# Optimization experiments

Hardware: AMD Instinct MI355X
Metric: run time of the kernel (lower is better)

## Reference

```python
import jax, jax.numpy as jnp
import numpy as np

B = 16384
D1 = 256
D2 = 256
D_FF = 1024
N_BINS = 16
TAIL = 3.0
MIN_VAL = 1e-3
MIN_TOTAL = N_BINS * MIN_VAL
TAIL_CONST = float(np.log(np.exp(1.0 - MIN_VAL) - 1.0))
D_OUT = (3 * N_BINS - 1) * D2  # 12032


def setup_inputs() -> dict:
    key = jax.random.key(0)
    ks = jax.random.split(key, 8)
    s = lambda fan: 1.0 / np.sqrt(fan)
    return {
        'x1': jax.random.normal(ks[0], (B, D1), jnp.float32),
        'x2': jax.random.normal(ks[1], (B, D2), jnp.float32),
        'W0': jax.random.normal(ks[2], (D1, D_FF), jnp.float32) * s(D1),
        'b0': jnp.zeros((D_FF,), jnp.float32),
        'W1': jax.random.normal(ks[3], (D_FF, D_FF), jnp.float32) * s(D_FF),
        'b1': jnp.zeros((D_FF,), jnp.float32),
        'W2': jax.random.normal(ks[4], (D_FF, D_OUT), jnp.float32) * s(D_FF),
        'b2': jnp.zeros((D_OUT,), jnp.float32),
    }


def _rqs_forward(x, wu, hu, du):
    # x: [B, D2]; wu, hu: [B, D2, N_BINS]; du: [B, D2, N_BINS-1]
    widths = MIN_VAL + (1.0 - MIN_TOTAL) * jax.nn.softmax(wu, axis=-1)
    heights = MIN_VAL + (1.0 - MIN_TOTAL) * jax.nn.softmax(hu, axis=-1)
    cw = jnp.cumsum(widths, axis=-1)
    cw = jnp.concatenate([jnp.zeros_like(cw[..., :1]), cw], axis=-1)
    cw = 2.0 * TAIL * cw - TAIL  # x bin edges in [-TAIL, TAIL], [B,D2,N_BINS+1]
    ch = jnp.cumsum(heights, axis=-1)
    ch = jnp.concatenate([jnp.zeros_like(ch[..., :1]), ch], axis=-1)
    ch = 2.0 * TAIL * ch - TAIL  # y bin edges
    w = cw[..., 1:] - cw[..., :-1]
    h = ch[..., 1:] - ch[..., :-1]
    # boundary derivatives padded so softplus(TAIL_CONST)+MIN_VAL == 1 (linear tails)
    pad = jnp.full_like(du[..., :1], TAIL_CONST)
    d = MIN_VAL + jax.nn.softplus(jnp.concatenate([pad, du, pad], axis=-1))  # [B,D2,N_BINS+1]
    inside = (x > -TAIL) & (x < TAIL)
    xc = jnp.clip(x, -TAIL, TAIL)
    # data-dependent bin search against interior edges
    idx = jnp.sum((xc[..., None] >= cw[..., 1:-1]).astype(jnp.int32), axis=-1)  # [B,D2]
    take = lambda a: jnp.take_along_axis(a, idx[..., None], axis=-1)[..., 0]
    xk = take(cw[..., :-1]); yk = take(ch[..., :-1])
    wk = take(w); hk = take(h)
    dk = take(d[..., :-1]); dk1 = take(d[..., 1:])
    sk = hk / wk
    theta = (xc - xk) / wk
    t1m = theta * (1.0 - theta)
    denom = sk + (dk + dk1 - 2.0 * sk) * t1m
    y = yk + hk * (sk * theta * theta + dk * t1m) / denom
    deriv = sk * sk * (dk1 * theta * theta + 2.0 * sk * t1m + dk * (1.0 - theta) ** 2) / (denom * denom)
    y = jnp.where(inside, y, x)            # identity tails
    logdet = jnp.where(inside, jnp.log(deriv), 0.0)
    return y, jnp.sum(logdet, axis=-1)     # [B,D2], [B]


def reference(x1, x2, W0, b0, W1, b1, W2, b2):
    # conditioner MLP: x1 -> spline parameters
    hdn = jax.nn.relu(x1 @ W0 + b0)
    hdn = jax.nn.relu(hdn @ W1 + b1)
    p = (hdn @ W2 + b2).reshape(-1, D2, 3 * N_BINS - 1)
    wu = p[..., :N_BINS]
    hu = p[..., N_BINS:2 * N_BINS]
    du = p[..., 2 * N_BINS:]
    y2, logdet = _rqs_forward(x2, wu, hu, du)
    return y2, logdet
```

## Files before the change

### kernel.cpp

```cpp
#include <hip/hip_runtime.h>
#include <math.h>

using u16 = unsigned short;
using bf16x8 = __attribute__((ext_vector_type(8))) short;
using f32x4  = __attribute__((ext_vector_type(4))) float;

#define DEV static __device__ __forceinline__

DEV u16 f2bf(float f) {
  union { float f; unsigned u; } v; v.f = f;
  unsigned u = v.u + 0x7fffu + ((v.u >> 16) & 1u);
  return (u16)(u >> 16);
}

DEV void gload16(const void* g, void* l) {
  __builtin_amdgcn_global_load_lds(
      (const __attribute__((address_space(1))) void*)g,
      (__attribute__((address_space(3))) void*)l, 16, 0, 0);
}

__global__ void k_conv_bf16(const float* __restrict__ in, u16* __restrict__ out, int n) {
  int i = blockIdx.x * 256 + threadIdx.x;
  if (i < n) out[i] = f2bf(in[i]);
}

__global__ void k_transconv(const float* __restrict__ in, u16* __restrict__ out,
                            int K, int Nin, int Nout, int pack) {
  __shared__ float t[32][33];
  int kb = blockIdx.x * 32, nb = blockIdx.y * 32;
  int tx = threadIdx.x & 31, ty = threadIdx.x >> 5;
  #pragma unroll
  for (int i = 0; i < 4; ++i) {
    int k = kb + ty + i * 8;
    int no = nb + tx;
    float v = 0.f;
    if (k < K && no < Nout) {
      if (pack) {
        int r = no % 48;
        if (r < 47) v = in[(size_t)k * Nin + (no / 48) * 47 + r];
      } else {
        v = in[(size_t)k * Nin + no];
      }
    }
    t[ty + i * 8][tx] = v;
  }
  __syncthreads();
  #pragma unroll
  for (int i = 0; i < 4; ++i) {
    int no = nb + ty + i * 8;
    int k = kb + tx;
    if (no < Nout && k < K) out[(size_t)no * K + k] = f2bf(t[tx][ty + i * 8]);
  }
}

__global__ __launch_bounds__(256)
void k_gemm_relu(const u16* __restrict__ A, const u16* __restrict__ Bt,
                 const float* __restrict__ bias, u16* __restrict__ C,
                 int N, int K) {
  constexpr int BM = 128, BN = 128, BK = 32;
  __shared__ __align__(16) u16 lds[(BM + BN) * BK];
  int tid = threadIdx.x, w = tid >> 6, lane = tid & 63;
  int bn = blockIdx.x, bm = blockIdx.y;
  int brow = bm * BM, bcol = bn * BN;
  int wm = w >> 1, wn = w & 1;
  int fr = lane & 15, fg = lane >> 4;
  f32x4 acc[4][4];
  #pragma unroll
  for (int i = 0; i < 4; ++i)
    #pragma unroll
    for (int j = 0; j < 4; ++j) acc[i][j] = (f32x4){0.f, 0.f, 0.f, 0.f};

  constexpr int ACH = BM * BK / 8;
  constexpr int CALLS = (BM + BN) * BK / 8 / 64;

  for (int kt = 0; kt < K; kt += BK) {
    for (int j = 0; j * 4 + w < CALLS; ++j) {
      int cb = (j * 4 + w) * 64;
      int c = cb + lane;
      const u16* g;
      if (c < ACH) {
        int row = c >> 2, c8 = c & 3;
        g = A + (size_t)(brow + row) * K + kt + c8 * 8;
      } else {
        int b = c - ACH;
        int nn = b >> 2, c8 = b & 3;
        g = Bt + (size_t)(bcol + nn) * K + kt + c8 * 8;
      }
      gload16(g, &lds[cb * 8]);
    }
    asm volatile("s_waitcnt vmcnt(0)" ::: "memory");
    __syncthreads();

    const u16* Al = lds;
    const u16* Bl = lds + BM * BK;
    bf16x8 af[4], bfr[4];
    #pragma unroll
    for (int mi = 0; mi < 4; ++mi)
      af[mi] = *(const bf16x8*)&Al[(wm * 64 + mi * 16 + fr) * BK + fg * 8];
    #pragma unroll
    for (int ni = 0; ni < 4; ++ni)
      bfr[ni] = *(const bf16x8*)&Bl[(wn * 64 + ni * 16 + fr) * BK + fg * 8];
    #pragma unroll
    for (int mi = 0; mi < 4; ++mi)
      #pragma unroll
      for (int ni = 0; ni < 4; ++ni)
        acc[mi][ni] = __builtin_amdgcn_mfma_f32_16x16x32_bf16(af[mi], bfr[ni], acc[mi][ni], 0, 0, 0);
    __syncthreads();
  }

  #pragma unroll
  for (int ni = 0; ni < 4; ++ni) {
    int col = bcol + wn * 64 + ni * 16 + fr;
    float bb = bias[col];
    #pragma unroll
    for (int mi = 0; mi < 4; ++mi) {
      #pragma unroll
      for (int q = 0; q < 4; ++q) {
        int row = brow + wm * 64 + mi * 16 + fg * 4 + q;
        float vv = acc[mi][ni][q] + bb;
        C[(size_t)row * N + col] = f2bf(vv > 0.f ? vv : 0.f);
      }
    }
  }
}

__global__ __launch_bounds__(256, 3)
void k_gemm3_fused(const u16* __restrict__ A, const u16* __restrict__ Bt,
                   const float* __restrict__ b2, const float* __restrict__ x2,
                   float* __restrict__ y2, float* __restrict__ ldpart) {
  extern __shared__ char smem[];
  const int tid = threadIdx.x, w = tid >> 6, lane = tid & 63;
  const int wm = w >> 1, wn = w & 1;
  const int fr = lane & 15, fg = lane >> 4;

  const int bid = blockIdx.x;
  const int bm = bid >> 6;
  const int bn = ((bid & 7) << 3) | ((bid >> 3) & 7);
  const int brow = bm * 128;

  const int csrc = (tid & 3) ^ ((tid >> 3) & 3);
  const u16* gA0 = A + (size_t)(brow + (tid >> 2)) * 1024 + csrc * 8;
  const u16* gB0 = Bt + (size_t)(bn * 192 + (tid >> 2)) * 1024 + csrc * 8;

#define ISSUE_ALL(t1) {                                               \
    const size_t ko_ = (size_t)(t1) * 32;                             \
    char* p_ = smem + ((t1) & 1) * 20480 + tid * 16;                  \
    gload16(gA0 + ko_, p_);                                           \
    gload16(gA0 + 65536 + ko_, p_ + 4096);                            \
    gload16(gB0 + ko_, p_ + 8192);                                    \
    gload16(gB0 + 65536 + ko_, p_ + 12288);                           \
    gload16(gB0 + 131072 + ko_, p_ + 16384); }

  const int sc = ((fg ^ ((fr >> 1) & 3)) << 4);

  f32x4 acc[4][6];
  #pragma unroll
  for (int m = 0; m < 4; ++m)
    #pragma unroll
    for (int n = 0; n < 6; ++n) acc[m][n] = (f32x4){0.f, 0.f, 0.f, 0.f};

  ISSUE_ALL(0);
  asm volatile("s_waitcnt vmcnt(0)" ::: "memory");
  __syncthreads();

  for (int t = 0; t < 32; ++t) {
    if (t < 31) ISSUE_ALL(t + 1);
    const char* Ab = smem + (t & 1) * 20480;
    const char* Bb = Ab + 8192;
    bf16x8 b[6];
    #pragma unroll
    for (int n = 0; n < 6; ++n)
      b[n] = *(const bf16x8*)(Bb + (wn * 96 + n * 16 + fr) * 64 + sc);
    __builtin_amdgcn_s_setprio(1);
    #pragma unroll
    for (int m = 0; m < 4; ++m) {
      bf16x8 a = *(const bf16x8*)(Ab + (wm * 64 + m * 16 + fr) * 64 + sc);
      #pragma unroll
      for (int n = 0; n < 6; ++n)
        acc[m][n] = __builtin_amdgcn_mfma_f32_16x16x32_bf16(a, b[n], acc[m][n], 0, 0, 0);
    }
    __builtin_amdgcn_s_setprio(0);
    asm volatile("s_waitcnt vmcnt(0)" ::: "memory");
    __syncthreads();
  }

  float* ldacc = (float*)(smem + 50176);
  float* fl = (float*)smem;
  #pragma unroll
  for (int rh = 0; rh < 2; ++rh) {
    if (wm == rh) {
      #pragma unroll
      for (int m = 0; m < 4; ++m)
        #pragma unroll
        for (int n = 0; n < 6; ++n) {
          const int g = wn * 2 + (n >= 3 ? 1 : 0);
          const int ci = (n % 3) * 16 + fr;
          #pragma unroll
          for (int q = 0; q < 4; ++q)
            fl[g * 3136 + (m * 16 + fg * 4 + q) * 49 + ci] = acc[m][n][q];
        }
    }
    __syncthreads();
    {
      const int g = tid >> 6, r = tid & 63;
      const float* pr = fl + g * 3136 + r * 49;
      const int grow = brow + rh * 64 + r;
      const int d2 = bn * 4 + g;
      const float* bb = b2 + (size_t)d2 * 47;

      float wv[16], hv[16];
      #pragma unroll
      for (int j = 0; j < 16; ++j) wv[j] = pr[j] + bb[j];
      #pragma unroll
      for (int j = 0; j < 16; ++j) hv[j] = pr[16 + j] + bb[16 + j];

      float x = x2[(size_t)grow * 256 + d2];
      float xc = fminf(fmaxf(x, -3.f), 3.f);

      float mw = wv[0];
      #pragma unroll
      for (int j = 1; j < 16; ++j) mw = fmaxf(mw, wv[j]);
      float sw = 0.f;
      #pragma unroll
      for (int j = 0; j < 16; ++j) { wv[j] = __expf(wv[j] - mw); sw += wv[j]; }
      float scw = 0.984f / sw;

      float mh = hv[0];
      #pragma unroll
      for (int j = 1; j < 16; ++j) mh = fmaxf(mh, hv[j]);
      float sh = 0.f;
      #pragma unroll
      for (int j = 0; j < 16; ++j) { hv[j] = __expf(hv[j] - mh); sh += hv[j]; }
      float sch = 0.984f / sh;

      int idx = 0;
      float xk = -3.f, cum = 0.f;
      #pragma unroll
      for (int i = 1; i <= 15; ++i) {
        cum += 0.001f + wv[i - 1] * scw;
        float cwi = 6.f * cum - 3.f;
        if (xc >= cwi) { idx = i; xk = cwi; }
      }
      float yk = -3.f, cumh = 0.f;
      #pragma unroll
      for (int i = 1; i <= 15; ++i) {
        cumh += 0.001f + hv[i - 1] * sch;
        float chi = 6.f * cumh - 3.f;
        if (i == idx) yk = chi;
      }
      float wk = 1.f, hk = 1.f;
      #pragma unroll
      for (int i = 0; i < 16; ++i) {
        if (i == idx) {
          wk = 6.f * (0.001f + wv[i] * scw);
          hk = 6.f * (0.001f + hv[i] * sch);
        }
      }
      float dk = 1.f, dk1 = 1.f;
      #pragma unroll
      for (int i = 1; i <= 15; ++i) {
        float u = pr[32 + i - 1] + bb[32 + i - 1];
        float e = __expf(u);
        float dd = 0.001f + (u > 15.f ? u : log1pf(e));
        if (i == idx) dk = dd;
        if (i == idx + 1) dk1 = dd;
      }

      float sk = hk / wk;
      float th = (xc - xk) / wk;
      float om = 1.f - th;
      float t1m = th * om;
      float den = sk + (dk + dk1 - 2.f * sk) * t1m;
      float y = yk + hk * (sk * th * th + dk * t1m) / den;
      float deriv = sk * sk * (dk1 * th * th + 2.f * sk * t1m + dk * om * om) / (den * den);
      bool inside = (x > -3.f) && (x < 3.f);
      float yout = inside ? y : x;
      float ld = inside ? __logf(deriv) : 0.f;

      y2[(size_t)grow * 256 + d2] = yout;
      ldacc[(rh * 64 + r) * 4 + g] = ld;
    }
    __syncthreads();
  }

  if (tid < 128) {
    float s = ldacc[tid * 4] + ldacc[tid * 4 + 1] + ldacc[tid * 4 + 2] + ldacc[tid * 4 + 3];
    ldpart[(size_t)bn * 16384 + brow + tid] = s;
  }
}

__global__ void k_reduce_ld(const float* __restrict__ part, float* __restrict__ out) {
  int r = blockIdx.x * 256 + threadIdx.x;
  float s = 0.f;
  for (int j = 0; j < 64; ++j) s += part[(size_t)j * 16384 + r];
  out[r] = s;
}

extern "C" void kernel_launch(void* const* d_in, const int* in_sizes, int n_in,
                              void* d_out, int out_size, void* d_ws, size_t ws_size,
                              hipStream_t stream) {
  const float* x1 = (const float*)d_in[0];
  const float* x2 = (const float*)d_in[1];
  const float* W0 = (const float*)d_in[2];
  const float* b0 = (const float*)d_in[3];
  const float* W1 = (const float*)d_in[4];
  const float* b1 = (const float*)d_in[5];
  const float* W2 = (const float*)d_in[6];
  const float* b2 = (const float*)d_in[7];
  float* y2 = (float*)d_out;
  float* logdet = y2 + (size_t)16384 * 256;

  char* ws = (char*)d_ws;
  u16* W2t = (u16*)ws;
  u16* W0t = (u16*)(ws + 25165824);
  u16* W1t = (u16*)(ws + 25165824 + 524288);
  u16* x1b = (u16*)(ws + 27787264);
  float* ldp = (float*)(ws + 27787264);
  u16* h1  = (u16*)(ws + 36175872);
  u16* h2  = (u16*)(ws + 69730304);

  hipFuncSetAttribute((const void*)k_gemm3_fused,
                      hipFuncAttributeMaxDynamicSharedMemorySize, 52224);

  k_conv_bf16<<<16384, 256, 0, stream>>>(x1, x1b, 16384 * 256);
  k_transconv<<<dim3(8, 32), 256, 0, stream>>>(W0, W0t, 256, 1024, 1024, 0);
  k_transconv<<<dim3(32, 32), 256, 0, stream>>>(W1, W1t, 1024, 1024, 1024, 0);
  k_transconv<<<dim3(32, 384), 256, 0, stream>>>(W2, W2t, 1024, 12032, 12288, 1);

  k_gemm_relu<<<dim3(8, 128), 256, 0, stream>>>(x1b, W0t, b0, h1, 1024, 256);
  k_gemm_relu<<<dim3(8, 128), 256, 0, stream>>>(h1, W1t, b1, h2, 1024, 1024);
  k_gemm3_fused<<<8192, 256, 52224, stream>>>(h2, W2t, b2, x2, y2, ldp);
  k_reduce_ld<<<64, 256, 0, stream>>>(ldp, logdet);
}
```

Measured before the change: 747.3 us.

## Triple-buffer the fused output GEMM main loop with partial vmcnt waits

Replaces the double-buffered K loop of the fused third GEMM with a three-stage LDS ring. Each step issues loads two tiles ahead and waits with vmcnt(5) instead of draining all outstanding loads, so global-to-LDS transfers overlap more with MFMA work. Raw s_barrier calls plus sched_barrier replace __syncthreads. LDS grows to 60KB and launch bounds drop from 3 to 2 blocks per CU, which trades occupancy for deeper prefetch.

```diff
diff --git a/kernel.cpp b/kernel.cpp
--- a/kernel.cpp
+++ b/kernel.cpp
@@ -124,7 +124,7 @@
   }
 }
 
-__global__ __launch_bounds__(256, 3)
+__global__ __launch_bounds__(256, 2)
 void k_gemm3_fused(const u16* __restrict__ A, const u16* __restrict__ Bt,
                    const float* __restrict__ b2, const float* __restrict__ x2,
                    float* __restrict__ y2, float* __restrict__ ldpart) {
@@ -142,9 +142,9 @@
   const u16* gA0 = A + (size_t)(brow + (tid >> 2)) * 1024 + csrc * 8;
   const u16* gB0 = Bt + (size_t)(bn * 192 + (tid >> 2)) * 1024 + csrc * 8;
 
-#define ISSUE_ALL(t1) {                                               \
+#define STAGE(t1, sb) {                                               \
     const size_t ko_ = (size_t)(t1) * 32;                             \
-    char* p_ = smem + ((t1) & 1) * 20480 + tid * 16;                  \
+    char* p_ = smem + (sb) + tid * 16;                                \
     gload16(gA0 + ko_, p_);                                           \
     gload16(gA0 + 65536 + ko_, p_ + 4096);                            \
     gload16(gB0 + ko_, p_ + 8192);                                    \
@@ -159,30 +159,39 @@
     #pragma unroll
     for (int n = 0; n < 6; ++n) acc[m][n] = (f32x4){0.f, 0.f, 0.f, 0.f};
 
-  ISSUE_ALL(0);
-  asm volatile("s_waitcnt vmcnt(0)" ::: "memory");
+#define COMPUTE(sb) {                                                 \
+    const char* Ab_ = smem + (sb);                                    \
+    const char* Bb_ = Ab_ + 8192;                                     \
+    bf16x8 b_[6];                                                     \
+    _Pragma("unroll")                                                 \
+    for (int n_ = 0; n_ < 6; ++n_)                                    \
+      b_[n_] = *(const bf16x8*)(Bb_ + (wn * 96 + n_ * 16 + fr) * 64 + sc); \
+    __builtin_amdgcn_s_setprio(1);                                    \
+    _Pragma("unroll")                                                 \
+    for (int m_ = 0; m_ < 4; ++m_) {                                  \
+      bf16x8 a_ = *(const bf16x8*)(Ab_ + (wm * 64 + m_ * 16 + fr) * 64 + sc); \
+      _Pragma("unroll")                                               \
+      for (int n_ = 0; n_ < 6; ++n_)                                  \
+        acc[m_][n_] = __builtin_amdgcn_mfma_f32_16x16x32_bf16(a_, b_[n_], acc[m_][n_], 0, 0, 0); \
+    }                                                                 \
+    __builtin_amdgcn_s_setprio(0); }
+
+#define VMW(n) { asm volatile("s_waitcnt vmcnt(" #n ")" ::: "memory"); \
+                 __builtin_amdgcn_sched_barrier(0); }
+#define RBAR() { __builtin_amdgcn_s_barrier(); __builtin_amdgcn_sched_barrier(0); }
+
+  STAGE(0, 0); STAGE(1, 20480);
+  VMW(5);
+  RBAR();
+
+  for (int j = 0; j < 10; ++j) {
+    STAGE(3 * j + 2, 40960); COMPUTE(0);     VMW(5); RBAR();
+    STAGE(3 * j + 3, 0);     COMPUTE(20480); VMW(5); RBAR();
+    STAGE(3 * j + 4, 20480); COMPUTE(40960); VMW(5); RBAR();
+  }
+  COMPUTE(0); VMW(0); RBAR();
+  COMPUTE(20480);
   __syncthreads();
-
-  for (int t = 0; t < 32; ++t) {
-    if (t < 31) ISSUE_ALL(t + 1);
-    const char* Ab = smem + (t & 1) * 20480;
-    const char* Bb = Ab + 8192;
-    bf16x8 b[6];
-    #pragma unroll
-    for (int n = 0; n < 6; ++n)
-      b[n] = *(const bf16x8*)(Bb + (wn * 96 + n * 16 + fr) * 64 + sc);
-    __builtin_amdgcn_s_setprio(1);
-    #pragma unroll
-    for (int m = 0; m < 4; ++m) {
-      bf16x8 a = *(const bf16x8*)(Ab + (wm * 64 + m * 16 + fr) * 64 + sc);
-      #pragma unroll
-      for (int n = 0; n < 6; ++n)
-        acc[m][n] = __builtin_amdgcn_mfma_f32_16x16x32_bf16(a, b[n], acc[m][n], 0, 0, 0);
-    }
-    __builtin_amdgcn_s_setprio(0);
-    asm volatile("s_waitcnt vmcnt(0)" ::: "memory");
-    __syncthreads();
-  }
 
   float* ldacc = (float*)(smem + 50176);
   float* fl = (float*)smem;
@@ -320,7 +329,7 @@
   u16* h2  = (u16*)(ws + 69730304);
 
   hipFuncSetAttribute((const void*)k_gemm3_fused,
-                      hipFuncAttributeMaxDynamicSharedMemorySize, 52224);
+                      hipFuncAttributeMaxDynamicSharedMemorySize, 61440);
 
   k_conv_bf16<<<16384, 256, 0, stream>>>(x1, x1b, 16384 * 256);
   k_transconv<<<dim3(8, 32), 256, 0, stream>>>(W0, W0t, 256, 1024, 1024, 0);
@@ -329,6 +338,6 @@
 
   k_gemm_relu<<<dim3(8, 128), 256, 0, stream>>>(x1b, W0t, b0, h1, 1024, 256);
   k_gemm_relu<<<dim3(8, 128), 256, 0, stream>>>(h1, W1t, b1, h2, 1024, 1024);
-  k_gemm3_fused<<<8192, 256, 52224, stream>>>(h2, W2t, b2, x2, y2, ldp);
+  k_gemm3_fused<<<8192, 256, 61440, stream>>>(h2, W2t, b2, x2, y2, ldp);
   k_reduce_ld<<<64, 256, 0, stream>>>(ldp, logdet);
 }
```

Measured after the change: 708.6 us. 1.05x faster.

## Enlarge fused GEMM3 tile to 256 rows with each warp owning all columns

Applied to the files above, without the earlier changes.

The fused final GEMM now computes a 256x192 tile per block instead of 128x192, with each of the four warps covering 64 rows and all 12 column fragments. This halves the grid and reuses each B tile across twice as many rows, cutting global/LDS traffic per MFMA. The cost is 48 accumulators per lane, which means more register pressure (launch bounds drop to 2 blocks per SM), more shared memory, and an epilogue that runs four serial row passes per block.

```diff
diff --git a/kernel.cpp b/kernel.cpp
--- a/kernel.cpp
+++ b/kernel.cpp
@@ -124,19 +124,18 @@
   }
 }
 
-__global__ __launch_bounds__(256, 3)
+__global__ __launch_bounds__(256, 2)
 void k_gemm3_fused(const u16* __restrict__ A, const u16* __restrict__ Bt,
                    const float* __restrict__ b2, const float* __restrict__ x2,
                    float* __restrict__ y2, float* __restrict__ ldpart) {
   extern __shared__ char smem[];
   const int tid = threadIdx.x, w = tid >> 6, lane = tid & 63;
-  const int wm = w >> 1, wn = w & 1;
   const int fr = lane & 15, fg = lane >> 4;
 
   const int bid = blockIdx.x;
   const int bm = bid >> 6;
   const int bn = ((bid & 7) << 3) | ((bid >> 3) & 7);
-  const int brow = bm * 128;
+  const int brow = bm * 256;
 
   const int csrc = (tid & 3) ^ ((tid >> 3) & 3);
   const u16* gA0 = A + (size_t)(brow + (tid >> 2)) * 1024 + csrc * 8;
@@ -144,20 +143,22 @@
 
 #define ISSUE_ALL(t1) {                                               \
     const size_t ko_ = (size_t)(t1) * 32;                             \
-    char* p_ = smem + ((t1) & 1) * 20480 + tid * 16;                  \
+    char* p_ = smem + ((t1) & 1) * 28672 + tid * 16;                  \
     gload16(gA0 + ko_, p_);                                           \
     gload16(gA0 + 65536 + ko_, p_ + 4096);                            \
-    gload16(gB0 + ko_, p_ + 8192);                                    \
-    gload16(gB0 + 65536 + ko_, p_ + 12288);                           \
-    gload16(gB0 + 131072 + ko_, p_ + 16384); }
+    gload16(gA0 + 131072 + ko_, p_ + 8192);                           \
+    gload16(gA0 + 196608 + ko_, p_ + 12288);                          \
+    gload16(gB0 + ko_, p_ + 16384);                                   \
+    gload16(gB0 + 65536 + ko_, p_ + 20480);                           \
+    gload16(gB0 + 131072 + ko_, p_ + 24576); }
 
   const int sc = ((fg ^ ((fr >> 1) & 3)) << 4);
 
-  f32x4 acc[4][6];
+  f32x4 acc[4][12];
   #pragma unroll
   for (int m = 0; m < 4; ++m)
     #pragma unroll
-    for (int n = 0; n < 6; ++n) acc[m][n] = (f32x4){0.f, 0.f, 0.f, 0.f};
+    for (int n = 0; n < 12; ++n) acc[m][n] = (f32x4){0.f, 0.f, 0.f, 0.f};
 
   ISSUE_ALL(0);
   asm volatile("s_waitcnt vmcnt(0)" ::: "memory");
@@ -165,46 +166,45 @@
 
   for (int t = 0; t < 32; ++t) {
     if (t < 31) ISSUE_ALL(t + 1);
-    const char* Ab = smem + (t & 1) * 20480;
-    const char* Bb = Ab + 8192;
-    bf16x8 b[6];
-    #pragma unroll
-    for (int n = 0; n < 6; ++n)
-      b[n] = *(const bf16x8*)(Bb + (wn * 96 + n * 16 + fr) * 64 + sc);
+    const char* Ab = smem + (t & 1) * 28672;
+    const char* Bb = Ab + 16384;
+    bf16x8 a[4];
+    #pragma unroll
+    for (int m = 0; m < 4; ++m)
+      a[m] = *(const bf16x8*)(Ab + (w * 64 + m * 16 + fr) * 64 + sc);
     __builtin_amdgcn_s_setprio(1);
     #pragma unroll
-    for (int m = 0; m < 4; ++m) {
-      bf16x8 a = *(const bf16x8*)(Ab + (wm * 64 + m * 16 + fr) * 64 + sc);
-      #pragma unroll
-      for (int n = 0; n < 6; ++n)
-        acc[m][n] = __builtin_amdgcn_mfma_f32_16x16x32_bf16(a, b[n], acc[m][n], 0, 0, 0);
+    for (int n = 0; n < 12; ++n) {
+      bf16x8 b = *(const bf16x8*)(Bb + (n * 16 + fr) * 64 + sc);
+      #pragma unroll
+      for (int m = 0; m < 4; ++m)
+        acc[m][n] = __builtin_amdgcn_mfma_f32_16x16x32_bf16(a[m], b, acc[m][n], 0, 0, 0);
     }
     __builtin_amdgcn_s_setprio(0);
     asm volatile("s_waitcnt vmcnt(0)" ::: "memory");
     __syncthreads();
   }
 
+  float* fl = (float*)smem;
   float* ldacc = (float*)(smem + 50176);
-  float* fl = (float*)smem;
-  #pragma unroll
-  for (int rh = 0; rh < 2; ++rh) {
-    if (wm == rh) {
+  #pragma unroll
+  for (int r = 0; r < 4; ++r) {
+    if (w == r) {
       #pragma unroll
       for (int m = 0; m < 4; ++m)
         #pragma unroll
-        for (int n = 0; n < 6; ++n) {
-          const int g = wn * 2 + (n >= 3 ? 1 : 0);
-          const int ci = (n % 3) * 16 + fr;
+        for (int n = 0; n < 12; ++n) {
+          const int g = n / 3, j = n % 3;
           #pragma unroll
           for (int q = 0; q < 4; ++q)
-            fl[g * 3136 + (m * 16 + fg * 4 + q) * 49 + ci] = acc[m][n][q];
+            fl[g * 3136 + (m * 16 + fg * 4 + q) * 49 + j * 16 + fr] = acc[m][n][q];
         }
     }
     __syncthreads();
     {
-      const int g = tid >> 6, r = tid & 63;
-      const float* pr = fl + g * 3136 + r * 49;
-      const int grow = brow + rh * 64 + r;
+      const int g = tid >> 6, rr = tid & 63;
+      const float* pr = fl + g * 3136 + rr * 49;
+      const int grow = brow + r * 64 + rr;
       const int d2 = bn * 4 + g;
       const float* bb = b2 + (size_t)d2 * 47;
 
@@ -278,14 +278,14 @@
       float ld = inside ? __logf(deriv) : 0.f;
 
       y2[(size_t)grow * 256 + d2] = yout;
-      ldacc[(rh * 64 + r) * 4 + g] = ld;
-    }
-    __syncthreads();
-  }
-
-  if (tid < 128) {
-    float s = ldacc[tid * 4] + ldacc[tid * 4 + 1] + ldacc[tid * 4 + 2] + ldacc[tid * 4 + 3];
-    ldpart[(size_t)bn * 16384 + brow + tid] = s;
+      ldacc[rr * 4 + g] = ld;
+    }
+    __syncthreads();
+    if (tid < 64) {
+      float s = ldacc[tid * 4] + ldacc[tid * 4 + 1] + ldacc[tid * 4 + 2] + ldacc[tid * 4 + 3];
+      ldpart[(size_t)bn * 16384 + brow + r * 64 + tid] = s;
+    }
+    __syncthreads();
   }
 }
 
@@ -320,7 +320,7 @@
   u16* h2  = (u16*)(ws + 69730304);
 
   hipFuncSetAttribute((const void*)k_gemm3_fused,
-                      hipFuncAttributeMaxDynamicSharedMemorySize, 52224);
+                      hipFuncAttributeMaxDynamicSharedMemorySize, 57344);
 
   k_conv_bf16<<<16384, 256, 0, stream>>>(x1, x1b, 16384 * 256);
   k_transconv<<<dim3(8, 32), 256, 0, stream>>>(W0, W0t, 256, 1024, 1024, 0);
@@ -329,6 +329,6 @@
 
   k_gemm_relu<<<dim3(8, 128), 256, 0, stream>>>(x1b, W0t, b0, h1, 1024, 256);
   k_gemm_relu<<<dim3(8, 128), 256, 0, stream>>>(h1, W1t, b1, h2, 1024, 1024);
-  k_gemm3_fused<<<8192, 256, 52224, stream>>>(h2, W2t, b2, x2, y2, ldp);
+  k_gemm3_fused<<<4096, 256, 57344, stream>>>(h2, W2t, b2, x2, y2, ldp);
   k_reduce_ld<<<64, 256, 0, stream>>>(ldp, logdet);
 }
```

New measurement: 863.4 us. +15.5%, slower.
